# Optimization experiments

Hardware: AMD Instinct MI355X
Metric: run time of the kernel (lower is better)

## Reference

```python
import jax, jax.numpy as jnp
import numpy as np

N, C = 262144, 128
BN_EPS = 1e-5


def setup_inputs() -> dict:
    key = jax.random.key(0)
    ks = jax.random.split(key, 9)
    s = 1.0 / np.sqrt(C)  # torch Linear default init scale
    return {
        "x": jax.random.normal(ks[0], (N, C), dtype=jnp.float32),
        "W1": jax.random.uniform(ks[1], (C, C), jnp.float32, -s, s),
        "b1": jax.random.uniform(ks[2], (C,), jnp.float32, -s, s),
        "gamma1": jnp.ones((C,), jnp.float32),
        "beta1": jnp.zeros((C,), jnp.float32),
        "W2": jax.random.uniform(ks[3], (C, C), jnp.float32, -s, s),
        "b2": jax.random.uniform(ks[4], (C,), jnp.float32, -s, s),
        "gamma2": jnp.ones((C,), jnp.float32),
        "beta2": jnp.zeros((C,), jnp.float32),
    }


def _batchnorm(h, gamma, beta):
    # training-mode BatchNorm1d: batch mean, biased variance, eps=1e-5
    m = jnp.mean(h, axis=0)
    v = jnp.var(h, axis=0)
    return (h - m) * jax.lax.rsqrt(v + BN_EPS) * gamma + beta


def reference(x, W1, b1, gamma1, beta1, W2, b2, gamma2, beta2):
    res = x
    out = x @ W1.T + b1
    # contextNormalization: only the in-place `d -= mean` loop has effect
    # (return value is discarded in the original), i.e. mean-center over batch
    out = out - jnp.mean(out, axis=0)
    out = jax.nn.relu(_batchnorm(out, gamma1, beta1))
    out = out @ W2.T + b2
    out = out - jnp.mean(out, axis=0)
    out = jax.nn.relu(_batchnorm(out, gamma2, beta2))
    return out + res
```

## Files before the change

### kernel.cpp

```cpp
#include <hip/hip_runtime.h>
#include <hip/hip_bf16.h>

#define NROWS 262144
#define CDIM  128
#define BN_EPS 1e-5f

typedef __attribute__((ext_vector_type(8))) short bf16x8;
typedef __attribute__((ext_vector_type(4))) float f32x4;

static __device__ __forceinline__ unsigned int f2bf_rtn(float f) {
  unsigned int u = __float_as_uint(f);
  return (u + 0x7fffu + ((u >> 16) & 1u)) >> 16;
}
static __device__ __forceinline__ float bf2f(unsigned int b) {
  return __uint_as_float(b << 16);
}

template <bool NORM>
__global__ void __launch_bounds__(256)
gemm_bn(const float* __restrict__ in, const float* __restrict__ W,
        const float* __restrict__ bias, const float* __restrict__ scsh,
        float* __restrict__ hout, float* __restrict__ stats)
{
  const int lane = threadIdx.x & 63;
  const int wave = threadIdx.x >> 6;
  const int l15  = lane & 15;
  const int lq   = lane >> 4;
  const int wcol = wave * 32;

  bf16x8 bh[2][4], bl[2][4];
#pragma unroll
  for (int jt = 0; jt < 2; ++jt) {
    const float* wrow = W + (wcol + jt * 16 + l15) * CDIM;
#pragma unroll
    for (int ks = 0; ks < 4; ++ks) {
      const int k0 = ks * 32 + lq * 8;
      float4 w0 = *(const float4*)(wrow + k0);
      float4 w1 = *(const float4*)(wrow + k0 + 4);
      float wv[8] = {w0.x, w0.y, w0.z, w0.w, w1.x, w1.y, w1.z, w1.w};
#pragma unroll
      for (int e = 0; e < 8; ++e) {
        unsigned int h = f2bf_rtn(wv[e]);
        bh[jt][ks][e] = (short)h;
        bl[jt][ks][e] = (short)f2bf_rtn(wv[e] - bf2f(h));
      }
    }
  }

  const float bias0 = bias[wcol + l15];
  const float bias1 = bias[wcol + 16 + l15];

  float s0 = 0.f, s1 = 0.f, q0 = 0.f, q1 = 0.f;

  const int NT = NROWS / 64;
  for (int t = blockIdx.x; t < NT; t += gridDim.x) {
#pragma unroll
    for (int rt = 0; rt < 4; ++rt) {
      const int r0 = t * 64 + rt * 16;
      f32x4 acc0 = {0.f, 0.f, 0.f, 0.f};
      f32x4 acc1 = {0.f, 0.f, 0.f, 0.f};
#pragma unroll
      for (int ks = 0; ks < 4; ++ks) {
        const int k0 = ks * 32 + lq * 8;
        const float* ap = in + (r0 + l15) * CDIM + k0;
        float4 a0 = *(const float4*)(ap);
        float4 a1 = *(const float4*)(ap + 4);
        float av[8] = {a0.x, a0.y, a0.z, a0.w, a1.x, a1.y, a1.z, a1.w};
        if constexpr (NORM) {
          float4 c0 = *(const float4*)(scsh + k0);
          float4 c1 = *(const float4*)(scsh + k0 + 4);
          float4 d0 = *(const float4*)(scsh + CDIM + k0);
          float4 d1 = *(const float4*)(scsh + CDIM + k0 + 4);
          float cv[8] = {c0.x, c0.y, c0.z, c0.w, c1.x, c1.y, c1.z, c1.w};
          float dv[8] = {d0.x, d0.y, d0.z, d0.w, d1.x, d1.y, d1.z, d1.w};
#pragma unroll
          for (int e = 0; e < 8; ++e)
            av[e] = fmaxf(av[e] * cv[e] + dv[e], 0.f);
        }
        bf16x8 ah, al;
#pragma unroll
        for (int e = 0; e < 8; ++e) {
          unsigned int h = f2bf_rtn(av[e]);
          ah[e] = (short)h;
          al[e] = (short)f2bf_rtn(av[e] - bf2f(h));
        }
        acc0 = __builtin_amdgcn_mfma_f32_16x16x32_bf16(al, bh[0][ks], acc0, 0, 0, 0);
        acc0 = __builtin_amdgcn_mfma_f32_16x16x32_bf16(ah, bl[0][ks], acc0, 0, 0, 0);
        acc0 = __builtin_amdgcn_mfma_f32_16x16x32_bf16(ah, bh[0][ks], acc0, 0, 0, 0);
        acc1 = __builtin_amdgcn_mfma_f32_16x16x32_bf16(al, bh[1][ks], acc1, 0, 0, 0);
        acc1 = __builtin_amdgcn_mfma_f32_16x16x32_bf16(ah, bl[1][ks], acc1, 0, 0, 0);
        acc1 = __builtin_amdgcn_mfma_f32_16x16x32_bf16(ah, bh[1][ks], acc1, 0, 0, 0);
      }
      if constexpr (NORM) __syncthreads();

      float* op = hout + (r0 + lq * 4) * CDIM + wcol + l15;
#pragma unroll
      for (int r = 0; r < 4; ++r) {
        float h0 = acc0[r] + bias0;
        float h1 = acc1[r] + bias1;
        s0 += h0; q0 += h0 * h0;
        s1 += h1; q1 += h1 * h1;
        op[r * CDIM] = h0;
        op[r * CDIM + 16] = h1;
      }
    }
  }

  s0 += __shfl_xor(s0, 16); s0 += __shfl_xor(s0, 32);
  s1 += __shfl_xor(s1, 16); s1 += __shfl_xor(s1, 32);
  q0 += __shfl_xor(q0, 16); q0 += __shfl_xor(q0, 32);
  q1 += __shfl_xor(q1, 16); q1 += __shfl_xor(q1, 32);
  if (lane < 16) {
    atomicAdd(&stats[wcol + lane],        s0);
    atomicAdd(&stats[wcol + 16 + lane],   s1);
    atomicAdd(&stats[CDIM + wcol + lane],      q0);
    atomicAdd(&stats[CDIM + wcol + 16 + lane], q1);
  }
}

__global__ void __launch_bounds__(128)
bn_coeffs(const float* __restrict__ stats, const float* __restrict__ gamma,
          const float* __restrict__ beta, float* __restrict__ scsh)
{
  const int c = threadIdx.x;
  const float inv_n = 1.0f / (float)NROWS;
  float m  = stats[c] * inv_n;
  float v  = stats[CDIM + c] * inv_n - m * m;
  float sc = gamma[c] * rsqrtf(v + BN_EPS);
  scsh[c]        = sc;
  scsh[CDIM + c] = beta[c] - m * sc;
}

__global__ void __launch_bounds__(256)
finalize(const float4* __restrict__ h2, const float4* __restrict__ xin,
         const float* __restrict__ scsh, float4* __restrict__ outp)
{
  const int n4 = NROWS * CDIM / 4;
  for (int i = blockIdx.x * blockDim.x + threadIdx.x; i < n4;
       i += gridDim.x * blockDim.x) {
    const int c0 = (i << 2) & (CDIM - 1);
    float4 h  = h2[i];
    float4 xv = xin[i];
    float4 sc = *(const float4*)(scsh + c0);
    float4 sh = *(const float4*)(scsh + CDIM + c0);
    float4 o;
    o.x = fmaxf(h.x * sc.x + sh.x, 0.f) + xv.x;
    o.y = fmaxf(h.y * sc.y + sh.y, 0.f) + xv.y;
    o.z = fmaxf(h.z * sc.z + sh.z, 0.f) + xv.z;
    o.w = fmaxf(h.w * sc.w + sh.w, 0.f) + xv.w;
    outp[i] = o;
  }
}

extern "C" void kernel_launch(void* const* d_in, const int* in_sizes, int n_in,
                              void* d_out, int out_size, void* d_ws, size_t ws_size,
                              hipStream_t stream) {
  (void)in_sizes; (void)n_in; (void)out_size; (void)ws_size;
  const float* x   = (const float*)d_in[0];
  const float* W1  = (const float*)d_in[1];
  const float* b1  = (const float*)d_in[2];
  const float* g1  = (const float*)d_in[3];
  const float* be1 = (const float*)d_in[4];
  const float* W2  = (const float*)d_in[5];
  const float* b2  = (const float*)d_in[6];
  const float* g2  = (const float*)d_in[7];
  const float* be2 = (const float*)d_in[8];

  float* hbuf   = (float*)d_out;
  float* stats1 = (float*)d_ws;
  float* stats2 = stats1 + 256;
  float* scsh1  = stats1 + 512;
  float* scsh2  = stats1 + 768;

  hipMemsetAsync(d_ws, 0, 2048, stream);

  gemm_bn<false><<<1024, 256, 0, stream>>>(x, W1, b1, nullptr, hbuf, stats1);
  bn_coeffs<<<1, 128, 0, stream>>>(stats1, g1, be1, scsh1);
  gemm_bn<true><<<1024, 256, 0, stream>>>(hbuf, W2, b2, scsh1, hbuf, stats2);
  bn_coeffs<<<1, 128, 0, stream>>>(stats2, g2, be2, scsh2);
  finalize<<<2048, 256, 0, stream>>>((const float4*)hbuf, (const float4*)x,
                                     scsh2, (float4*)d_out);
}
```

Baseline: 486.1 us.

## Stage the shared A tile in LDS as bf16 hi/lo with double-buffered prefetch

Previously each of the four waves loaded the same 16x128 input rows from global memory and did the split-bf16 conversion (plus BN+ReLU in the second GEMM) separately, repeating that work four times. Now all 256 threads cooperatively load one 16-row slab, convert it once into hi/lo bf16 planes in LDS, and prefetch the next slab while MFMAs run on the current buffer. Each block handles a contiguous range of rows, and the launch bounds request occupancy 4. The finalize kernel now handles two float4s per thread with nontemporal stores and launches twice as many blocks. The cost is LDS use and a barrier per slab.

Result: faster. 430.1 us (-11.5%).

```diff
diff --git a/kernel.cpp b/kernel.cpp
--- a/kernel.cpp
+++ b/kernel.cpp
@@ -4,9 +4,12 @@
 #define NROWS 262144
 #define CDIM  128
 #define BN_EPS 1e-5f
+#define GGRID 1024
+#define SPB   (NROWS / 16 / GGRID)
 
 typedef __attribute__((ext_vector_type(8))) short bf16x8;
 typedef __attribute__((ext_vector_type(4))) float f32x4;
+#define LROW 136
 
 static __device__ __forceinline__ unsigned int f2bf_rtn(float f) {
   unsigned int u = __float_as_uint(f);
@@ -17,16 +20,21 @@
 }
 
 template <bool NORM>
-__global__ void __launch_bounds__(256)
+__global__ void __launch_bounds__(256, 4)
 gemm_bn(const float* __restrict__ in, const float* __restrict__ W,
         const float* __restrict__ bias, const float* __restrict__ scsh,
         float* __restrict__ hout, float* __restrict__ stats)
 {
-  const int lane = threadIdx.x & 63;
-  const int wave = threadIdx.x >> 6;
+  __shared__ __align__(16) short lds[2][2][16][LROW];
+
+  const int tid  = threadIdx.x;
+  const int lane = tid & 63;
+  const int wave = tid >> 6;
   const int l15  = lane & 15;
   const int lq   = lane >> 4;
   const int wcol = wave * 32;
+  const int srow = tid >> 4;
+  const int sk0  = (tid & 15) * 8;
 
   bf16x8 bh[2][4], bl[2][4];
 #pragma unroll
@@ -35,9 +43,9 @@
 #pragma unroll
     for (int ks = 0; ks < 4; ++ks) {
       const int k0 = ks * 32 + lq * 8;
-      float4 w0 = *(const float4*)(wrow + k0);
-      float4 w1 = *(const float4*)(wrow + k0 + 4);
-      float wv[8] = {w0.x, w0.y, w0.z, w0.w, w1.x, w1.y, w1.z, w1.w};
+      f32x4 w0 = *(const f32x4*)(wrow + k0);
+      f32x4 w1 = *(const f32x4*)(wrow + k0 + 4);
+      float wv[8] = {w0.x,w0.y,w0.z,w0.w,w1.x,w1.y,w1.z,w1.w};
 #pragma unroll
       for (int e = 0; e < 8; ++e) {
         unsigned int h = f2bf_rtn(wv[e]);
@@ -47,62 +55,86 @@
     }
   }
 
+  float scv[8], shv[8];
+  if constexpr (NORM) {
+#pragma unroll
+    for (int e = 0; e < 8; ++e) {
+      scv[e] = scsh[sk0 + e];
+      shv[e] = scsh[CDIM + sk0 + e];
+    }
+  }
+
   const float bias0 = bias[wcol + l15];
   const float bias1 = bias[wcol + 16 + l15];
-
   float s0 = 0.f, s1 = 0.f, q0 = 0.f, q1 = 0.f;
 
-  const int NT = NROWS / 64;
-  for (int t = blockIdx.x; t < NT; t += gridDim.x) {
-#pragma unroll
-    for (int rt = 0; rt < 4; ++rt) {
-      const int r0 = t * 64 + rt * 16;
-      f32x4 acc0 = {0.f, 0.f, 0.f, 0.f};
-      f32x4 acc1 = {0.f, 0.f, 0.f, 0.f};
-#pragma unroll
-      for (int ks = 0; ks < 4; ++ks) {
-        const int k0 = ks * 32 + lq * 8;
-        const float* ap = in + (r0 + l15) * CDIM + k0;
-        float4 a0 = *(const float4*)(ap);
-        float4 a1 = *(const float4*)(ap + 4);
-        float av[8] = {a0.x, a0.y, a0.z, a0.w, a1.x, a1.y, a1.z, a1.w};
-        if constexpr (NORM) {
-          float4 c0 = *(const float4*)(scsh + k0);
-          float4 c1 = *(const float4*)(scsh + k0 + 4);
-          float4 d0 = *(const float4*)(scsh + CDIM + k0);
-          float4 d1 = *(const float4*)(scsh + CDIM + k0 + 4);
-          float cv[8] = {c0.x, c0.y, c0.z, c0.w, c1.x, c1.y, c1.z, c1.w};
-          float dv[8] = {d0.x, d0.y, d0.z, d0.w, d1.x, d1.y, d1.z, d1.w};
-#pragma unroll
-          for (int e = 0; e < 8; ++e)
-            av[e] = fmaxf(av[e] * cv[e] + dv[e], 0.f);
-        }
-        bf16x8 ah, al;
-#pragma unroll
-        for (int e = 0; e < 8; ++e) {
-          unsigned int h = f2bf_rtn(av[e]);
-          ah[e] = (short)h;
-          al[e] = (short)f2bf_rtn(av[e] - bf2f(h));
-        }
-        acc0 = __builtin_amdgcn_mfma_f32_16x16x32_bf16(al, bh[0][ks], acc0, 0, 0, 0);
-        acc0 = __builtin_amdgcn_mfma_f32_16x16x32_bf16(ah, bl[0][ks], acc0, 0, 0, 0);
-        acc0 = __builtin_amdgcn_mfma_f32_16x16x32_bf16(ah, bh[0][ks], acc0, 0, 0, 0);
-        acc1 = __builtin_amdgcn_mfma_f32_16x16x32_bf16(al, bh[1][ks], acc1, 0, 0, 0);
-        acc1 = __builtin_amdgcn_mfma_f32_16x16x32_bf16(ah, bl[1][ks], acc1, 0, 0, 0);
-        acc1 = __builtin_amdgcn_mfma_f32_16x16x32_bf16(ah, bh[1][ks], acc1, 0, 0, 0);
-      }
-      if constexpr (NORM) __syncthreads();
-
-      float* op = hout + (r0 + lq * 4) * CDIM + wcol + l15;
-#pragma unroll
-      for (int r = 0; r < 4; ++r) {
-        float h0 = acc0[r] + bias0;
-        float h1 = acc1[r] + bias1;
-        s0 += h0; q0 += h0 * h0;
-        s1 += h1; q1 += h1 * h1;
-        op[r * CDIM] = h0;
-        op[r * CDIM + 16] = h1;
-      }
+  const int row0 = blockIdx.x * (SPB * 16);
+
+  auto cvt_write = [&](int buf, f32x4 g0, f32x4 g1) {
+    float av[8] = {g0.x,g0.y,g0.z,g0.w,g1.x,g1.y,g1.z,g1.w};
+    if constexpr (NORM) {
+#pragma unroll
+      for (int e = 0; e < 8; ++e)
+        av[e] = fmaxf(av[e] * scv[e] + shv[e], 0.f);
+    }
+    bf16x8 hi, lo;
+#pragma unroll
+    for (int e = 0; e < 8; ++e) {
+      unsigned int h = f2bf_rtn(av[e]);
+      hi[e] = (short)h;
+      lo[e] = (short)f2bf_rtn(av[e] - bf2f(h));
+    }
+    *(bf16x8*)&lds[buf][0][srow][sk0] = hi;
+    *(bf16x8*)&lds[buf][1][srow][sk0] = lo;
+  };
+
+  {
+    const float* ap = in + (size_t)(row0 + srow) * CDIM + sk0;
+    f32x4 g0 = *(const f32x4*)ap;
+    f32x4 g1 = *(const f32x4*)(ap + 4);
+    cvt_write(0, g0, g1);
+  }
+  __syncthreads();
+
+  for (int s = 0; s < SPB; ++s) {
+    const int cur = s & 1;
+    const int r0 = row0 + s * 16;
+
+    f32x4 g0 = {0,0,0,0}, g1 = {0,0,0,0};
+    const bool more = (s + 1 < SPB);
+    if (more) {
+      const float* ap = in + (size_t)(r0 + 16 + srow) * CDIM + sk0;
+      g0 = *(const f32x4*)ap;
+      g1 = *(const f32x4*)(ap + 4);
+    }
+
+    f32x4 acc0 = {0.f,0.f,0.f,0.f};
+    f32x4 acc1 = {0.f,0.f,0.f,0.f};
+#pragma unroll
+    for (int ks = 0; ks < 4; ++ks) {
+      const int kc = ks * 32 + lq * 8;
+      bf16x8 ah = *(const bf16x8*)&lds[cur][0][l15][kc];
+      bf16x8 al = *(const bf16x8*)&lds[cur][1][l15][kc];
+      acc0 = __builtin_amdgcn_mfma_f32_16x16x32_bf16(al, bh[0][ks], acc0, 0, 0, 0);
+      acc0 = __builtin_amdgcn_mfma_f32_16x16x32_bf16(ah, bl[0][ks], acc0, 0, 0, 0);
+      acc0 = __builtin_amdgcn_mfma_f32_16x16x32_bf16(ah, bh[0][ks], acc0, 0, 0, 0);
+      acc1 = __builtin_amdgcn_mfma_f32_16x16x32_bf16(al, bh[1][ks], acc1, 0, 0, 0);
+      acc1 = __builtin_amdgcn_mfma_f32_16x16x32_bf16(ah, bl[1][ks], acc1, 0, 0, 0);
+      acc1 = __builtin_amdgcn_mfma_f32_16x16x32_bf16(ah, bh[1][ks], acc1, 0, 0, 0);
+    }
+
+    if (more) cvt_write(cur ^ 1, g0, g1);
+    __syncthreads();
+
+    float* op = hout + (size_t)(r0 + lq * 4) * CDIM + wcol + l15;
+#pragma unroll
+    for (int r = 0; r < 4; ++r) {
+      float h0 = acc0[r] + bias0;
+      float h1 = acc1[r] + bias1;
+      s0 += h0; q0 += h0 * h0;
+      s1 += h1; q1 += h1 * h1;
+      op[r * CDIM] = h0;
+      op[r * CDIM + 16] = h1;
     }
   }
 
@@ -111,8 +143,8 @@
   q0 += __shfl_xor(q0, 16); q0 += __shfl_xor(q0, 32);
   q1 += __shfl_xor(q1, 16); q1 += __shfl_xor(q1, 32);
   if (lane < 16) {
-    atomicAdd(&stats[wcol + lane],        s0);
-    atomicAdd(&stats[wcol + 16 + lane],   s1);
+    atomicAdd(&stats[wcol + lane],             s0);
+    atomicAdd(&stats[wcol + 16 + lane],        s1);
     atomicAdd(&stats[CDIM + wcol + lane],      q0);
     atomicAdd(&stats[CDIM + wcol + 16 + lane], q1);
   }
@@ -132,23 +164,30 @@
 }
 
 __global__ void __launch_bounds__(256)
-finalize(const float4* __restrict__ h2, const float4* __restrict__ xin,
-         const float* __restrict__ scsh, float4* __restrict__ outp)
+finalize(const f32x4* __restrict__ h2, const f32x4* __restrict__ xin,
+         const float* __restrict__ scsh, f32x4* __restrict__ outp)
 {
   const int n4 = NROWS * CDIM / 4;
-  for (int i = blockIdx.x * blockDim.x + threadIdx.x; i < n4;
-       i += gridDim.x * blockDim.x) {
+  const int stride = gridDim.x * blockDim.x * 2;
+  for (int i = (blockIdx.x * blockDim.x + threadIdx.x) * 2; i < n4; i += stride) {
+    f32x4 hA = h2[i], hB = h2[i + 1];
+    f32x4 xA = xin[i], xB = xin[i + 1];
     const int c0 = (i << 2) & (CDIM - 1);
-    float4 h  = h2[i];
-    float4 xv = xin[i];
-    float4 sc = *(const float4*)(scsh + c0);
-    float4 sh = *(const float4*)(scsh + CDIM + c0);
-    float4 o;
-    o.x = fmaxf(h.x * sc.x + sh.x, 0.f) + xv.x;
-    o.y = fmaxf(h.y * sc.y + sh.y, 0.f) + xv.y;
-    o.z = fmaxf(h.z * sc.z + sh.z, 0.f) + xv.z;
-    o.w = fmaxf(h.w * sc.w + sh.w, 0.f) + xv.w;
-    outp[i] = o;
+    f32x4 scA = *(const f32x4*)(scsh + c0);
+    f32x4 scB = *(const f32x4*)(scsh + c0 + 4);
+    f32x4 shA = *(const f32x4*)(scsh + CDIM + c0);
+    f32x4 shB = *(const f32x4*)(scsh + CDIM + c0 + 4);
+    f32x4 oA, oB;
+    oA.x = fmaxf(hA.x * scA.x + shA.x, 0.f) + xA.x;
+    oA.y = fmaxf(hA.y * scA.y + shA.y, 0.f) + xA.y;
+    oA.z = fmaxf(hA.z * scA.z + shA.z, 0.f) + xA.z;
+    oA.w = fmaxf(hA.w * scA.w + shA.w, 0.f) + xA.w;
+    oB.x = fmaxf(hB.x * scB.x + shB.x, 0.f) + xB.x;
+    oB.y = fmaxf(hB.y * scB.y + shB.y, 0.f) + xB.y;
+    oB.z = fmaxf(hB.z * scB.z + shB.z, 0.f) + xB.z;
+    oB.w = fmaxf(hB.w * scB.w + shB.w, 0.f) + xB.w;
+    __builtin_nontemporal_store(oA, &outp[i]);
+    __builtin_nontemporal_store(oB, &outp[i + 1]);
   }
 }
 
@@ -172,12 +211,12 @@
   float* scsh1  = stats1 + 512;
   float* scsh2  = stats1 + 768;
 
-  hipMemsetAsync(d_ws, 0, 2048, stream);
-
-  gemm_bn<false><<<1024, 256, 0, stream>>>(x, W1, b1, nullptr, hbuf, stats1);
+  (void)hipMemsetAsync(d_ws, 0, 2048, stream);
+
+  gemm_bn<false><<<GGRID, 256, 0, stream>>>(x, W1, b1, nullptr, hbuf, stats1);
   bn_coeffs<<<1, 128, 0, stream>>>(stats1, g1, be1, scsh1);
-  gemm_bn<true><<<1024, 256, 0, stream>>>(hbuf, W2, b2, scsh1, hbuf, stats2);
+  gemm_bn<true><<<GGRID, 256, 0, stream>>>(hbuf, W2, b2, scsh1, hbuf, stats2);
   bn_coeffs<<<1, 128, 0, stream>>>(stats2, g2, be2, scsh2);
-  finalize<<<2048, 256, 0, stream>>>((const float4*)hbuf, (const float4*)x,
-                                     scsh2, (float4*)d_out);
-}
+  finalize<<<4096, 256, 0, stream>>>((const f32x4*)hbuf, (const f32x4*)x,
+                                     scsh2, (f32x4*)d_out);
+}
```
